# Performance work log

Measured on AMD Instinct MI355X. Metric: run time of the kernel, lower is better.

Reference implementation:

```python
import jax, jax.numpy as jnp
import numpy as np

NEG_SLOPE = 0.2

def setup_inputs() -> dict:
    key = jax.random.key(0)
    k1, k2, k3, k4 = jax.random.split(key, 4)
    bs, n, f_in, f_out, n_head = 8, 2048, 64, 32, 4
    h = jax.random.normal(k1, (bs, n, f_in), dtype=jnp.float32)
    # xavier_uniform-like scales (exact init values irrelevant for correctness baseline)
    w = jax.random.normal(k2, (n_head, f_in, f_out), dtype=jnp.float32) * 0.14
    a_src = jax.random.normal(k3, (n_head, f_out, 1), dtype=jnp.float32) * 0.3
    a_dst = jax.random.normal(k4, (n_head, f_out, 1), dtype=jnp.float32) * 0.3
    b = jnp.zeros((f_out,), dtype=jnp.float32)
    return {"h": h, "w": w, "a_src": a_src, "a_dst": a_dst, "b": b}

def reference(h, w, a_src, a_dst, b):
    # h: [bs, n, f_in]; w: [H, f_in, f_out]
    h_prime = jnp.einsum('bnf,hfo->bhno', h, w)            # [bs, H, n, f_out]
    attn_src = jnp.einsum('bhno,hot->bhnt', h_prime, a_src)  # [bs, H, n, 1]
    attn_dst = jnp.einsum('bhno,hot->bhnt', h_prime, a_dst)  # [bs, H, n, 1]
    # additive broadcast: score[b,h,i,j] = src[i] + dst[j]
    attn = attn_src + jnp.swapaxes(attn_dst, -1, -2)        # [bs, H, n, n]
    attn = jnp.where(attn >= 0, attn, NEG_SLOPE * attn)     # leaky relu
    attn = jax.nn.softmax(attn, axis=-1)
    # dropout p=0.0 -> identity
    output = jnp.einsum('bhnm,bhmo->bhno', attn, h_prime) + b
    return (output, attn)
```

## Files before the change

kernel.cpp:

```cpp
#include <hip/hip_runtime.h>
#include <hip/hip_bf16.h>

#define NSLOPE 0.2f

typedef __bf16 bf16x8 __attribute__((ext_vector_type(8)));
typedef float  f32x4  __attribute__((ext_vector_type(4)));

__device__ __forceinline__ float lrelu(float x) { return x >= 0.f ? x : NSLOPE * x; }

__global__ __launch_bounds__(256) void k_hprime(
    const float* __restrict__ hg,
    const float* __restrict__ wg,
    const float* __restrict__ a_src,
    const float* __restrict__ a_dst,
    __hip_bfloat16* __restrict__ hpT,
    float* __restrict__ srcv,
    float* __restrict__ dstv)
{
    __shared__ float w_lds[64 * 32];
    __shared__ float h_lds[64 * 64];
    __shared__ __hip_bfloat16 t_lds[32 * 72];

    const int t  = threadIdx.x;
    const int bh = blockIdx.x >> 5;
    const int n0 = (blockIdx.x & 31) * 64;
    const int b  = bh >> 2, hh = bh & 3;

    {
        const float4* s4 = (const float4*)(wg + hh * 2048);
        float4* d4 = (float4*)w_lds;
        d4[t] = s4[t];
        d4[t + 256] = s4[t + 256];
        const float4* s4h = (const float4*)(hg + ((size_t)(b * 2048 + n0)) * 64);
        float4* d4h = (float4*)h_lds;
#pragma unroll
        for (int k = 0; k < 4; k++) d4h[t + 256 * k] = s4h[t + 256 * k];
    }
    __syncthreads();

    const int o  = t & 31;
    const int nb = t >> 5;
    float acc[8];
#pragma unroll
    for (int k = 0; k < 8; k++) acc[k] = 0.f;
    for (int f = 0; f < 64; f++) {
        const float wv = w_lds[f * 32 + o];
#pragma unroll
        for (int k = 0; k < 8; k++)
            acc[k] = fmaf(h_lds[(nb + 8 * k) * 64 + f], wv, acc[k]);
    }
    const float as = a_src[hh * 32 + o];
    const float ad = a_dst[hh * 32 + o];
#pragma unroll
    for (int k = 0; k < 8; k++) {
        float sv = acc[k] * as;
        float dv = acc[k] * ad;
#pragma unroll
        for (int m = 16; m >= 1; m >>= 1) {
            sv += __shfl_xor(sv, m);
            dv += __shfl_xor(dv, m);
        }
        if (o == 0) {
            const int n = n0 + nb + 8 * k;
            srcv[bh * 2048 + n] = sv;
            dstv[bh * 2048 + n] = dv;
        }
    }
#pragma unroll
    for (int k = 0; k < 8; k++)
        t_lds[o * 72 + nb + 8 * k] = __float2bfloat16(acc[k]);
    __syncthreads();
    {
        const int oo = t >> 3;
        const int ch = t & 7;
        const uint4 v = *(const uint4*)(&t_lds[oo * 72 + ch * 8]);
        *(uint4*)(hpT + ((size_t)(bh * 32 + oo)) * 2048 + n0 + ch * 8) = v;
    }
}

__global__ __launch_bounds__(256) void k_attn(
    const __hip_bfloat16* __restrict__ hpT,
    const float* __restrict__ srcv,
    const float* __restrict__ dstv,
    const float* __restrict__ bias,
    float* __restrict__ outp,
    float* __restrict__ attn)
{
    __shared__ float dst_lds[2048];
    __shared__ float src_lds[64];
    __shared__ float m_lds[64];
    __shared__ float is_lds[64];
    __shared__ float red_lds[4];
    __shared__ char  hp_lds[8192];
    __shared__ char  p_lds[16384];

    const int t    = threadIdx.x;
    const int bh   = blockIdx.x >> 5;
    const int row0 = (blockIdx.x & 31) * 64;

    float lmax = -1e30f;
    {
        const float4* s4 = (const float4*)(dstv + bh * 2048);
        float4* d4 = (float4*)dst_lds;
#pragma unroll
        for (int k = 0; k < 2; k++) {
            const float4 v = s4[t + 256 * k];
            d4[t + 256 * k] = v;
            lmax = fmaxf(lmax, fmaxf(fmaxf(v.x, v.y), fmaxf(v.z, v.w)));
        }
    }
    if (t < 64) src_lds[t] = srcv[bh * 2048 + row0 + t];
#pragma unroll
    for (int m = 32; m >= 1; m >>= 1) lmax = fmaxf(lmax, __shfl_xor(lmax, m));
    if ((t & 63) == 0) red_lds[t >> 6] = lmax;
    __syncthreads();
    const float dmax = fmaxf(fmaxf(red_lds[0], red_lds[1]), fmaxf(red_lds[2], red_lds[3]));

    {
        const int r = t >> 2, q = t & 3;
        const float sr  = src_lds[r];
        const float m_r = lrelu(sr + dmax);
        float s = 0.f;
        for (int it = 0; it < 128; it++) {
            const float4 dv = *(const float4*)(dst_lds + q * 4 + 16 * it);
            s += __expf(lrelu(sr + dv.x) - m_r);
            s += __expf(lrelu(sr + dv.y) - m_r);
            s += __expf(lrelu(sr + dv.z) - m_r);
            s += __expf(lrelu(sr + dv.w) - m_r);
        }
        s += __shfl_xor(s, 1);
        s += __shfl_xor(s, 2);
        if (q == 0) { m_lds[r] = m_r; is_lds[r] = 1.f / s; }
    }
    __syncthreads();

    f32x4 acc0 = {0.f, 0.f, 0.f, 0.f};
    f32x4 acc1 = {0.f, 0.f, 0.f, 0.f};
    const int wv_ = t >> 6;
    const int l   = t & 63;
    const int lr  = l & 15;
    const int g   = l >> 4;

    for (int tile = 0; tile < 16; tile++) {
        const int j0 = tile * 128;
#pragma unroll
        for (int k = 0; k < 2; k++) {
            const int c    = t + 256 * k;
            const int oo   = c >> 4;
            const int slot = c & 15;
            const uint4 v = *(const uint4*)(hpT + ((size_t)(bh * 32 + oo)) * 2048 + j0 + slot * 8);
            const int jl = slot * 8;
            const int j5 = jl >> 5, jj = jl & 31;
            const int pos = ((jj & 12) << 1) + ((jj & 16) >> 2);
            char* base = hp_lds + oo * 256;
            const int sa1 = (j5 * 4 + (pos >> 3)) ^ (oo & 15);
            const int bi1 = (pos & 7) * 2;
            const int pos2 = pos + 8;
            const int sa2 = (j5 * 4 + (pos2 >> 3)) ^ (oo & 15);
            const int bi2 = (pos2 & 7) * 2;
            const unsigned long long lo = ((unsigned long long)v.y << 32) | (unsigned long long)v.x;
            const unsigned long long hi = ((unsigned long long)v.w << 32) | (unsigned long long)v.z;
            *(unsigned long long*)(base + (sa1 << 4) + bi1) = lo;
            *(unsigned long long*)(base + (sa2 << 4) + bi2) = hi;
        }
        {
            const int jl = (t & 31) * 4;
            const int rB = (t >> 5) * 8;
            const int j5 = jl >> 5, jj = jl & 31;
            const int pos = ((jj & 12) << 1) + (jj & 3) + ((jj & 16) >> 2);
            const int sa = j5 * 4 + (pos >> 3);
            const int bi = (pos & 7) * 2;
            const float4 dj = *(const float4*)(dst_lds + j0 + jl);
#pragma unroll
            for (int k = 0; k < 8; k++) {
                const int r = rB + k;
                const float sr   = src_lds[r];
                const float m_r  = m_lds[r];
                const float is_r = is_lds[r];
                f32x4 p;
                p[0] = __expf(lrelu(sr + dj.x) - m_r) * is_r;
                p[1] = __expf(lrelu(sr + dj.y) - m_r) * is_r;
                p[2] = __expf(lrelu(sr + dj.z) - m_r) * is_r;
                p[3] = __expf(lrelu(sr + dj.w) - m_r) * is_r;
                __builtin_nontemporal_store(p,
                    (f32x4*)(attn + ((size_t)(bh * 2048) + row0 + r) * 2048 + j0 + jl));
                union { __hip_bfloat16 hb[4]; unsigned long long u; } pk;
                pk.hb[0] = __float2bfloat16(p[0]);
                pk.hb[1] = __float2bfloat16(p[1]);
                pk.hb[2] = __float2bfloat16(p[2]);
                pk.hb[3] = __float2bfloat16(p[3]);
                *(unsigned long long*)(p_lds + r * 256 + ((sa ^ (r & 15)) << 4) + bi) = pk.u;
            }
        }
        __syncthreads();
        {
            const char* prow  = p_lds + (wv_ * 16 + lr) * 256;
            const char* hrow0 = hp_lds + lr * 256;
            const char* hrow1 = hp_lds + (16 + lr) * 256;
#pragma unroll
            for (int ks = 0; ks < 4; ks++) {
                const int sidx = (((ks * 4 + g) ^ lr) << 4);
                const bf16x8 a  = *(const bf16x8*)(prow + sidx);
                const bf16x8 b0 = *(const bf16x8*)(hrow0 + sidx);
                const bf16x8 b1 = *(const bf16x8*)(hrow1 + sidx);
                acc0 = __builtin_amdgcn_mfma_f32_16x16x32_bf16(a, b0, acc0, 0, 0, 0);
                acc1 = __builtin_amdgcn_mfma_f32_16x16x32_bf16(a, b1, acc1, 0, 0, 0);
            }
        }
        __syncthreads();
    }
    {
        const float b0 = bias[lr];
        const float b1 = bias[16 + lr];
#pragma unroll
        for (int reg = 0; reg < 4; reg++) {
            const int grow = row0 + wv_ * 16 + g * 4 + reg;
            float* op = outp + ((size_t)(bh * 2048) + grow) * 32;
            op[lr]      = acc0[reg] + b0;
            op[16 + lr] = acc1[reg] + b1;
        }
    }
}

extern "C" void kernel_launch(void* const* d_in, const int* in_sizes, int n_in,
                              void* d_out, int out_size, void* d_ws, size_t ws_size,
                              hipStream_t stream) {
    (void)in_sizes; (void)n_in; (void)out_size; (void)ws_size;
    const float* h     = (const float*)d_in[0];
    const float* w     = (const float*)d_in[1];
    const float* a_src = (const float*)d_in[2];
    const float* a_dst = (const float*)d_in[3];
    const float* b     = (const float*)d_in[4];

    float* out  = (float*)d_out;
    float* attn = out + (size_t)8 * 4 * 2048 * 32;

    __hip_bfloat16* hpT = (__hip_bfloat16*)d_ws;
    float* srcv = (float*)((char*)d_ws + (size_t)32 * 32 * 2048 * 2);
    float* dstv = srcv + 32 * 2048;

    k_hprime<<<1024, 256, 0, stream>>>(h, w, a_src, a_dst, hpT, srcv, dstv);
    k_attn  <<<1024, 256, 0, stream>>>(hpT, srcv, dstv, b, out, attn);
}
```

Measured before the change: 146.8 us.

## Factor softmax exponentials per column and split attention write from PV matmul

Scores are pre-scaled by log2(e). exp(lrelu(s+d)-m) is factored into a per-row factor times a per-column exp2(d) or exp2(0.2d), so each block precomputes the packed bf16 column exponentials once and a row needs only a select and a multiply. Blocks are split into two roles: one writes the fp32 attention matrix, the other rebuilds bf16 P in registers and runs the MFMA PV product straight from global hp, with hp stored in an MFMA-friendly permuted layout. This removes most per-element exp work and the LDS staging and barriers of the old tile loop. In exchange P is computed twice, grid size doubles, and the column exponentials are rounded to bf16, which also lowers the precision of the stored fp32 attention.

Result: no change. 147.8 us (+0.7%).

```diff
diff --git a/kernel.cpp b/kernel.cpp
--- a/kernel.cpp
+++ b/kernel.cpp
@@ -1,19 +1,38 @@
 #include <hip/hip_runtime.h>
 #include <hip/hip_bf16.h>
 
-#define NSLOPE 0.2f
-
 typedef __bf16 bf16x8 __attribute__((ext_vector_type(8)));
 typedef float  f32x4  __attribute__((ext_vector_type(4)));
 
-__device__ __forceinline__ float lrelu(float x) { return x >= 0.f ? x : NSLOPE * x; }
+#define LOG2E 1.4426950408889634f
+
+__device__ __forceinline__ float lrelu(float x) { return x >= 0.f ? x : 0.2f * x; }
+
+__device__ __forceinline__ float exp2f_fast(float x) {
+#if __has_builtin(__builtin_amdgcn_exp2f)
+    return __builtin_amdgcn_exp2f(x);
+#else
+    return __expf(x * 0.6931471805599453f);
+#endif
+}
+
+__device__ __forceinline__ unsigned short bfbits(float x) {
+    __hip_bfloat16 h = __float2bfloat16(x);
+    return *reinterpret_cast<unsigned short*>(&h);
+}
+
+__device__ __forceinline__ unsigned packE(float d) {
+    const unsigned b1 = bfbits(exp2f_fast(d));
+    const unsigned b2 = bfbits(exp2f_fast(0.2f * d));
+    return (b1 << 16) | b2;
+}
 
 __global__ __launch_bounds__(256) void k_hprime(
     const float* __restrict__ hg,
     const float* __restrict__ wg,
     const float* __restrict__ a_src,
     const float* __restrict__ a_dst,
-    __hip_bfloat16* __restrict__ hpT,
+    __hip_bfloat16* __restrict__ hpF,
     float* __restrict__ srcv,
     float* __restrict__ dstv)
 {
@@ -49,8 +68,8 @@
         for (int k = 0; k < 8; k++)
             acc[k] = fmaf(h_lds[(nb + 8 * k) * 64 + f], wv, acc[k]);
     }
-    const float as = a_src[hh * 32 + o];
-    const float ad = a_dst[hh * 32 + o];
+    const float as = a_src[hh * 32 + o] * LOG2E;
+    const float ad = a_dst[hh * 32 + o] * LOG2E;
 #pragma unroll
     for (int k = 0; k < 8; k++) {
         float sv = acc[k] * as;
@@ -73,35 +92,38 @@
     {
         const int oo = t >> 3;
         const int ch = t & 7;
-        const uint4 v = *(const uint4*)(&t_lds[oo * 72 + ch * 8]);
-        *(uint4*)(hpT + ((size_t)(bh * 32 + oo)) * 2048 + n0 + ch * 8) = v;
-    }
-}
-
-__global__ __launch_bounds__(256) void k_attn(
-    const __hip_bfloat16* __restrict__ hpT,
+        const int jb = ch >> 2, g = ch & 3;
+        const __hip_bfloat16* src0 = &t_lds[oo * 72 + jb * 32 + g * 4];
+        union { unsigned long long q[2]; uint4 v; } u;
+        u.q[0] = *(const unsigned long long*)(src0);
+        u.q[1] = *(const unsigned long long*)(src0 + 16);
+        *(uint4*)(hpF + ((size_t)(bh * 32 + oo)) * 2048 + n0 + ch * 8) = u.v;
+    }
+}
+
+__global__ __launch_bounds__(256) void k_main(
+    const __hip_bfloat16* __restrict__ hpF,
     const float* __restrict__ srcv,
     const float* __restrict__ dstv,
     const float* __restrict__ bias,
     float* __restrict__ outp,
     float* __restrict__ attn)
 {
-    __shared__ float dst_lds[2048];
-    __shared__ float src_lds[64];
-    __shared__ float m_lds[64];
-    __shared__ float is_lds[64];
-    __shared__ float red_lds[4];
-    __shared__ char  hp_lds[8192];
-    __shared__ char  p_lds[16384];
+    __shared__ __attribute__((aligned(16))) float    d_lds[2048];
+    __shared__ __attribute__((aligned(16))) unsigned e12[2048];
+    __shared__ float ns_lds[64], a1_lds[64], a2_lds[64];
+    __shared__ float red[4];
 
     const int t    = threadIdx.x;
-    const int bh   = blockIdx.x >> 5;
-    const int row0 = (blockIdx.x & 31) * 64;
+    const int role = blockIdx.x & 1;
+    const int wid  = blockIdx.x >> 1;
+    const int bh   = wid >> 5;
+    const int row0 = (wid & 31) * 64;
 
     float lmax = -1e30f;
     {
         const float4* s4 = (const float4*)(dstv + bh * 2048);
-        float4* d4 = (float4*)dst_lds;
+        float4* d4 = (float4*)d_lds;
 #pragma unroll
         for (int k = 0; k < 2; k++) {
             const float4 v = s4[t + 256 * k];
@@ -109,115 +131,105 @@
             lmax = fmaxf(lmax, fmaxf(fmaxf(v.x, v.y), fmaxf(v.z, v.w)));
         }
     }
-    if (t < 64) src_lds[t] = srcv[bh * 2048 + row0 + t];
 #pragma unroll
     for (int m = 32; m >= 1; m >>= 1) lmax = fmaxf(lmax, __shfl_xor(lmax, m));
-    if ((t & 63) == 0) red_lds[t >> 6] = lmax;
-    __syncthreads();
-    const float dmax = fmaxf(fmaxf(red_lds[0], red_lds[1]), fmaxf(red_lds[2], red_lds[3]));
+    if ((t & 63) == 0) red[t >> 6] = lmax;
+    __syncthreads();
+    const float dmax = fmaxf(fmaxf(red[0], red[1]), fmaxf(red[2], red[3]));
+
+    {
+#pragma unroll
+        for (int k = 0; k < 2; k++) {
+            const float4 dv = *((const float4*)d_lds + t + 256 * k);
+            uint4 u;
+            u.x = packE(dv.x); u.y = packE(dv.y);
+            u.z = packE(dv.z); u.w = packE(dv.w);
+            *((uint4*)e12 + t + 256 * k) = u;
+        }
+    }
+    __syncthreads();
 
     {
         const int r = t >> 2, q = t & 3;
-        const float sr  = src_lds[r];
-        const float m_r = lrelu(sr + dmax);
-        float s = 0.f;
+        const float s  = srcv[bh * 2048 + row0 + r];
+        const float ns = -s;
+        float acc1 = 0.f, acc2 = 0.f;
         for (int it = 0; it < 128; it++) {
-            const float4 dv = *(const float4*)(dst_lds + q * 4 + 16 * it);
-            s += __expf(lrelu(sr + dv.x) - m_r);
-            s += __expf(lrelu(sr + dv.y) - m_r);
-            s += __expf(lrelu(sr + dv.z) - m_r);
-            s += __expf(lrelu(sr + dv.w) - m_r);
-        }
-        s += __shfl_xor(s, 1);
-        s += __shfl_xor(s, 2);
-        if (q == 0) { m_lds[r] = m_r; is_lds[r] = 1.f / s; }
-    }
-    __syncthreads();
-
-    f32x4 acc0 = {0.f, 0.f, 0.f, 0.f};
-    f32x4 acc1 = {0.f, 0.f, 0.f, 0.f};
-    const int wv_ = t >> 6;
-    const int l   = t & 63;
-    const int lr  = l & 15;
-    const int g   = l >> 4;
-
-    for (int tile = 0; tile < 16; tile++) {
-        const int j0 = tile * 128;
-#pragma unroll
-        for (int k = 0; k < 2; k++) {
-            const int c    = t + 256 * k;
-            const int oo   = c >> 4;
-            const int slot = c & 15;
-            const uint4 v = *(const uint4*)(hpT + ((size_t)(bh * 32 + oo)) * 2048 + j0 + slot * 8);
-            const int jl = slot * 8;
-            const int j5 = jl >> 5, jj = jl & 31;
-            const int pos = ((jj & 12) << 1) + ((jj & 16) >> 2);
-            char* base = hp_lds + oo * 256;
-            const int sa1 = (j5 * 4 + (pos >> 3)) ^ (oo & 15);
-            const int bi1 = (pos & 7) * 2;
-            const int pos2 = pos + 8;
-            const int sa2 = (j5 * 4 + (pos2 >> 3)) ^ (oo & 15);
-            const int bi2 = (pos2 & 7) * 2;
-            const unsigned long long lo = ((unsigned long long)v.y << 32) | (unsigned long long)v.x;
-            const unsigned long long hi = ((unsigned long long)v.w << 32) | (unsigned long long)v.z;
-            *(unsigned long long*)(base + (sa1 << 4) + bi1) = lo;
-            *(unsigned long long*)(base + (sa2 << 4) + bi2) = hi;
-        }
-        {
-            const int jl = (t & 31) * 4;
-            const int rB = (t >> 5) * 8;
-            const int j5 = jl >> 5, jj = jl & 31;
-            const int pos = ((jj & 12) << 1) + (jj & 3) + ((jj & 16) >> 2);
-            const int sa = j5 * 4 + (pos >> 3);
-            const int bi = (pos & 7) * 2;
-            const float4 dj = *(const float4*)(dst_lds + j0 + jl);
-#pragma unroll
-            for (int k = 0; k < 8; k++) {
-                const int r = rB + k;
-                const float sr   = src_lds[r];
-                const float m_r  = m_lds[r];
-                const float is_r = is_lds[r];
+            const int j = q * 4 + it * 16;
+            const float4 dv = *(const float4*)(d_lds + j);
+            const uint4  uv = *(const uint4*)(e12 + j);
+            { const bool c = dv.x >= ns; acc1 += c ? __uint_as_float(uv.x & 0xffff0000u) : 0.f; acc2 += c ? 0.f : __uint_as_float(uv.x << 16); }
+            { const bool c = dv.y >= ns; acc1 += c ? __uint_as_float(uv.y & 0xffff0000u) : 0.f; acc2 += c ? 0.f : __uint_as_float(uv.y << 16); }
+            { const bool c = dv.z >= ns; acc1 += c ? __uint_as_float(uv.z & 0xffff0000u) : 0.f; acc2 += c ? 0.f : __uint_as_float(uv.z << 16); }
+            { const bool c = dv.w >= ns; acc1 += c ? __uint_as_float(uv.w & 0xffff0000u) : 0.f; acc2 += c ? 0.f : __uint_as_float(uv.w << 16); }
+        }
+        acc1 += __shfl_xor(acc1, 1); acc1 += __shfl_xor(acc1, 2);
+        acc2 += __shfl_xor(acc2, 1); acc2 += __shfl_xor(acc2, 2);
+        if (q == 0) {
+            const float m  = lrelu(s + dmax);
+            const float f1 = exp2f_fast(s - m);
+            const float f2 = exp2f_fast(0.2f * s - m);
+            const float is = 1.f / (f1 * acc1 + f2 * acc2);
+            ns_lds[r] = ns; a1_lds[r] = f1 * is; a2_lds[r] = f2 * is;
+        }
+    }
+    __syncthreads();
+
+    if (role == 0) {
+        float* rowbase = attn + ((size_t)(bh * 2048) + row0) * 2048;
+        for (int r = 0; r < 64; r++) {
+            const float ns = ns_lds[r], a1 = a1_lds[r], a2 = a2_lds[r];
+            float* rp = rowbase + (size_t)r * 2048;
+#pragma unroll
+            for (int h2 = 0; h2 < 2; h2++) {
+                const int j = t * 4 + h2 * 1024;
+                const float4 dv = *(const float4*)(d_lds + j);
+                const uint4  uv = *(const uint4*)(e12 + j);
                 f32x4 p;
-                p[0] = __expf(lrelu(sr + dj.x) - m_r) * is_r;
-                p[1] = __expf(lrelu(sr + dj.y) - m_r) * is_r;
-                p[2] = __expf(lrelu(sr + dj.z) - m_r) * is_r;
-                p[3] = __expf(lrelu(sr + dj.w) - m_r) * is_r;
-                __builtin_nontemporal_store(p,
-                    (f32x4*)(attn + ((size_t)(bh * 2048) + row0 + r) * 2048 + j0 + jl));
-                union { __hip_bfloat16 hb[4]; unsigned long long u; } pk;
-                pk.hb[0] = __float2bfloat16(p[0]);
-                pk.hb[1] = __float2bfloat16(p[1]);
-                pk.hb[2] = __float2bfloat16(p[2]);
-                pk.hb[3] = __float2bfloat16(p[3]);
-                *(unsigned long long*)(p_lds + r * 256 + ((sa ^ (r & 15)) << 4) + bi) = pk.u;
+                { const bool c = dv.x >= ns; p[0] = (c ? a1 : a2) * __uint_as_float(c ? (uv.x & 0xffff0000u) : (uv.x << 16)); }
+                { const bool c = dv.y >= ns; p[1] = (c ? a1 : a2) * __uint_as_float(c ? (uv.y & 0xffff0000u) : (uv.y << 16)); }
+                { const bool c = dv.z >= ns; p[2] = (c ? a1 : a2) * __uint_as_float(c ? (uv.z & 0xffff0000u) : (uv.z << 16)); }
+                { const bool c = dv.w >= ns; p[3] = (c ? a1 : a2) * __uint_as_float(c ? (uv.w & 0xffff0000u) : (uv.w << 16)); }
+                __builtin_nontemporal_store(p, (f32x4*)(rp + j));
             }
         }
-        __syncthreads();
-        {
-            const char* prow  = p_lds + (wv_ * 16 + lr) * 256;
-            const char* hrow0 = hp_lds + lr * 256;
-            const char* hrow1 = hp_lds + (16 + lr) * 256;
-#pragma unroll
-            for (int ks = 0; ks < 4; ks++) {
-                const int sidx = (((ks * 4 + g) ^ lr) << 4);
-                const bf16x8 a  = *(const bf16x8*)(prow + sidx);
-                const bf16x8 b0 = *(const bf16x8*)(hrow0 + sidx);
-                const bf16x8 b1 = *(const bf16x8*)(hrow1 + sidx);
-                acc0 = __builtin_amdgcn_mfma_f32_16x16x32_bf16(a, b0, acc0, 0, 0, 0);
-                acc1 = __builtin_amdgcn_mfma_f32_16x16x32_bf16(a, b1, acc1, 0, 0, 0);
-            }
-        }
-        __syncthreads();
-    }
-    {
-        const float b0 = bias[lr];
-        const float b1 = bias[16 + lr];
+    } else {
+        const int l  = t & 63, w = t >> 6;
+        const int lr = l & 15, g = l >> 4;
+        const int rA = w * 16 + lr;
+        const float ns = ns_lds[rA], a1 = a1_lds[rA], a2 = a2_lds[rA];
+        const __hip_bfloat16* hb0 = hpF + ((size_t)(bh * 32 + lr)) * 2048;
+        const __hip_bfloat16* hb1 = hpF + ((size_t)(bh * 32 + 16 + lr)) * 2048;
+        f32x4 acc0 = {0.f, 0.f, 0.f, 0.f};
+        f32x4 acc1v = {0.f, 0.f, 0.f, 0.f};
+        for (int jb = 0; jb < 64; jb++) {
+            const int j = jb * 32 + g * 4;
+            const float4 dA = *(const float4*)(d_lds + j);
+            const float4 dB = *(const float4*)(d_lds + j + 16);
+            const uint4  uA = *(const uint4*)(e12 + j);
+            const uint4  uB = *(const uint4*)(e12 + j + 16);
+            union { unsigned short us[8]; bf16x8 v; } A;
+            { const bool c = dA.x >= ns; A.us[0] = bfbits((c ? a1 : a2) * __uint_as_float(c ? (uA.x & 0xffff0000u) : (uA.x << 16))); }
+            { const bool c = dA.y >= ns; A.us[1] = bfbits((c ? a1 : a2) * __uint_as_float(c ? (uA.y & 0xffff0000u) : (uA.y << 16))); }
+            { const bool c = dA.z >= ns; A.us[2] = bfbits((c ? a1 : a2) * __uint_as_float(c ? (uA.z & 0xffff0000u) : (uA.z << 16))); }
+            { const bool c = dA.w >= ns; A.us[3] = bfbits((c ? a1 : a2) * __uint_as_float(c ? (uA.w & 0xffff0000u) : (uA.w << 16))); }
+            { const bool c = dB.x >= ns; A.us[4] = bfbits((c ? a1 : a2) * __uint_as_float(c ? (uB.x & 0xffff0000u) : (uB.x << 16))); }
+            { const bool c = dB.y >= ns; A.us[5] = bfbits((c ? a1 : a2) * __uint_as_float(c ? (uB.y & 0xffff0000u) : (uB.y << 16))); }
+            { const bool c = dB.z >= ns; A.us[6] = bfbits((c ? a1 : a2) * __uint_as_float(c ? (uB.z & 0xffff0000u) : (uB.z << 16))); }
+            { const bool c = dB.w >= ns; A.us[7] = bfbits((c ? a1 : a2) * __uint_as_float(c ? (uB.w & 0xffff0000u) : (uB.w << 16))); }
+            const bf16x8 b0 = *(const bf16x8*)(hb0 + jb * 32 + g * 8);
+            const bf16x8 b1 = *(const bf16x8*)(hb1 + jb * 32 + g * 8);
+            acc0  = __builtin_amdgcn_mfma_f32_16x16x32_bf16(A.v, b0, acc0, 0, 0, 0);
+            acc1v = __builtin_amdgcn_mfma_f32_16x16x32_bf16(A.v, b1, acc1v, 0, 0, 0);
+        }
+        const float b0v = bias[lr];
+        const float b1v = bias[16 + lr];
 #pragma unroll
         for (int reg = 0; reg < 4; reg++) {
-            const int grow = row0 + wv_ * 16 + g * 4 + reg;
+            const int grow = row0 + w * 16 + g * 4 + reg;
             float* op = outp + ((size_t)(bh * 2048) + grow) * 32;
-            op[lr]      = acc0[reg] + b0;
-            op[16 + lr] = acc1[reg] + b1;
+            op[lr]      = acc0[reg] + b0v;
+            op[16 + lr] = acc1v[reg] + b1v;
         }
     }
 }
@@ -235,10 +247,10 @@
     float* out  = (float*)d_out;
     float* attn = out + (size_t)8 * 4 * 2048 * 32;
 
-    __hip_bfloat16* hpT = (__hip_bfloat16*)d_ws;
+    __hip_bfloat16* hpF = (__hip_bfloat16*)d_ws;
     float* srcv = (float*)((char*)d_ws + (size_t)32 * 32 * 2048 * 2);
     float* dstv = srcv + 32 * 2048;
 
-    k_hprime<<<1024, 256, 0, stream>>>(h, w, a_src, a_dst, hpT, srcv, dstv);
-    k_attn  <<<1024, 256, 0, stream>>>(hpT, srcv, dstv, b, out, attn);
-}
+    k_hprime<<<1024, 256, 0, stream>>>(h, w, a_src, a_dst, hpF, srcv, dstv);
+    k_main  <<<2048, 256, 0, stream>>>(hpF, srcv, dstv, b, out, attn);
+}
```
